# Performance work log

Measured on AMD Instinct MI355X. Metric: run time of the kernel, lower is better.

Reference implementation:

```python
import jax, jax.numpy as jnp
import numpy as np

C = 64
DQK = C // 8  # 8
B, H, W = 1, 128, 128


def setup_inputs() -> dict:
    key = jax.random.key(0)
    ks = jax.random.split(key, 8)
    s = 0.05
    return {
        "x": jax.random.normal(ks[0], (B, C, H, W), dtype=jnp.float32),
        "Wq": jax.random.normal(ks[1], (DQK, C), dtype=jnp.float32) * s,
        "bq": jnp.zeros((DQK,), dtype=jnp.float32),
        "Wk": jax.random.normal(ks[2], (DQK, C), dtype=jnp.float32) * s,
        "bk": jnp.zeros((DQK,), dtype=jnp.float32),
        "Wv": jax.random.normal(ks[3], (C, C), dtype=jnp.float32) * s,
        "bv": jnp.zeros((C,), dtype=jnp.float32),
        "gamma": jnp.ones((1,), dtype=jnp.float32),  # torch inits to 0; nonzero for testing
    }


def reference(x, Wq, bq, Wk, bk, Wv, bv, gamma):
    b, c, h, w = x.shape
    n = h * w
    xf = x.reshape(b, c, n)                      # [B,C,N] (unfold k=1 == reshape)
    q = jnp.einsum('dc,bcn->bnd', Wq, xf) + bq   # [B,N,DQK]
    k = jnp.einsum('dc,bcn->bnd', Wk, xf) + bk   # [B,N,DQK]
    v = jnp.einsum('dc,bcn->bnd', Wv, xf) + bv   # [B,N,C]
    attn = jnp.einsum('bnd,bmd->bnm', q, k)      # [B,N,N] (no scaling, as in source)
    attn = jax.nn.softmax(attn, axis=-1)
    out = jnp.einsum('bnm,bmc->bnc', attn, v)    # [B,N,C]
    out = out.transpose(0, 2, 1).reshape(b, c, h, w)  # fold k=1 == reshape
    return gamma * out + x
```

## Files before the change

kernel.cpp:

```cpp
#include <hip/hip_runtime.h>
#include <stdint.h>

#define NTOK 16384

typedef __attribute__((ext_vector_type(8))) short short8;
typedef __attribute__((ext_vector_type(4))) float f32x4;
typedef __attribute__((ext_vector_type(16))) float f32x16;

__device__ __forceinline__ short f2bf_rne(float f) {
  union { float f; unsigned u; } a; a.f = f;
  unsigned r = a.u + 0x7fffu + ((a.u >> 16) & 1u);
  return (short)(r >> 16);
}

__device__ __forceinline__ float fast_exp2(float x) {
#if __has_builtin(__builtin_amdgcn_exp2f)
  return __builtin_amdgcn_exp2f(x);
#else
  return exp2f(x);
#endif
}

__device__ __forceinline__ unsigned pack_rn(float lo, float hi) {
  union { float f; unsigned u; } a, b;
  a.f = lo; b.f = hi;
  return __builtin_amdgcn_perm(b.u + 0x8000u, a.u + 0x8000u, 0x07060302u);
}

__device__ __forceinline__ int sigma32(int s) {
  int t = (s >> 2) & 3;
  return (t == 1 || t == 2) ? (s ^ 12) : s;
}

__global__ __launch_bounds__(256) void proj_qk_kernel(
    const float* __restrict__ x,
    const float* __restrict__ Wq, const float* __restrict__ bq,
    const float* __restrict__ Wk, const float* __restrict__ bk,
    short* __restrict__ Qp, short* __restrict__ Kp)
{
  __shared__ float sWq[512], sWk[512], sbq[8], sbk[8];
  const int tid = threadIdx.x;
  for (int i = tid; i < 512; i += 256) { sWq[i] = Wq[i]; sWk[i] = Wk[i]; }
  if (tid < 8) { sbq[tid] = bq[tid]; sbk[tid] = bk[tid]; }
  __syncthreads();

  const int n = blockIdx.x * 256 + tid;
  float xv[64];
#pragma unroll
  for (int c = 0; c < 64; ++c) xv[c] = x[c * NTOK + n];

  short8 qv, kv;
#pragma unroll
  for (int d = 0; d < 8; ++d) {
    float qa = sbq[d], ka = sbk[d];
#pragma unroll
    for (int c = 0; c < 64; c += 4) {
      f32x4 wq = *reinterpret_cast<const f32x4*>(&sWq[d * 64 + c]);
      f32x4 wk = *reinterpret_cast<const f32x4*>(&sWk[d * 64 + c]);
      qa += wq[0]*xv[c] + wq[1]*xv[c+1] + wq[2]*xv[c+2] + wq[3]*xv[c+3];
      ka += wk[0]*xv[c] + wk[1]*xv[c+1] + wk[2]*xv[c+2] + wk[3]*xv[c+3];
    }
    qv[d] = f2bf_rne(qa);
    kv[d] = f2bf_rne(ka * 1.44269504f);
  }
  *reinterpret_cast<short8*>(Qp + (size_t)n * 8) = qv;
  const int slot = (n & ~31) | sigma32(n & 31);
  *reinterpret_cast<short8*>(Kp + (size_t)slot * 8) = kv;
}

__global__ __launch_bounds__(256) void proj_v_kernel(
    const float* __restrict__ x,
    const float* __restrict__ Wv, const float* __restrict__ bv,
    short* __restrict__ VF)
{
  __shared__ float sW[64 * 65];
  __shared__ float sx[64][32];
  __shared__ float sb[64];
  const int tid = threadIdx.x;
  const int n0 = blockIdx.x * 32;

  for (int i = tid; i < 4096; i += 256) sW[(i >> 6) * 65 + (i & 63)] = Wv[i];
  if (tid < 64) sb[tid] = bv[tid];
  for (int i = tid; i < 2048; i += 256) {
    const int r = i >> 5, col = i & 31;
    sx[r][col] = x[(size_t)r * NTOK + n0 + col];
  }
  __syncthreads();

  const int c   = tid & 63;
  const int oct = tid >> 6;

  float v[8];
  const float bias = sb[c];
#pragma unroll
  for (int j = 0; j < 8; ++j) v[j] = bias;

  for (int cp = 0; cp < 64; ++cp) {
    const float wv = sW[c * 65 + cp];
    const float* xr = &sx[cp][oct * 8];
#pragma unroll
    for (int j = 0; j < 8; ++j) v[j] += wv * xr[j];
  }

  const int n    = n0 + oct * 8;
  const int frag = (n >> 4) * 2 + (c >> 5);
  const int lane = ((n >> 3) & 1) * 32 + (c & 31);
  short8 ov;
#pragma unroll
  for (int j = 0; j < 8; ++j) ov[j] = f2bf_rne(v[j]);
  *reinterpret_cast<short8*>(VF + (size_t)frag * 512 + lane * 8) = ov;
}

__global__ __launch_bounds__(512, 4) void attn_fused_kernel(
    const short* __restrict__ Qp, const short* __restrict__ Kp,
    const short* __restrict__ VF,
    const float* __restrict__ x, const float* __restrict__ gamma,
    float* __restrict__ out)
{
  __shared__ float lacc[8 * 2080];
  __shared__ float slsum[8 * 32];

  const int tid  = threadIdx.x;
  const int w    = tid >> 6;
  const int lane = tid & 63;
  const int hi   = lane >> 5;
  const int ln   = lane & 31;
  const int q0   = blockIdx.x * 32;

  const short8 zero8 = {0,0,0,0,0,0,0,0};
  f32x16 zf16;
#pragma unroll
  for (int i = 0; i < 16; ++i) zf16[i] = 0.f;

  short8 qf = hi ? zero8
                 : *reinterpret_cast<const short8*>(Qp + (size_t)(q0 + ln) * 8);

  f32x16 acc0 = zf16, acc1 = zf16;
  float lsum = 0.f;

  const int kvlen = NTOK / 8;
  const int kv_lo = w * kvlen;
  const int nh    = kvlen / 32;

  const short* KP0 = Kp + ((size_t)kv_lo + ln) * 8;
  const short* VF0 = VF + (size_t)kv_lo * 64 + lane * 8;

  auto loadK = [&](int h, short8& kf) {
    kf = *reinterpret_cast<const short8*>(KP0 + (size_t)h * 256);
  };
  auto loadV = [&](int h, short8 (&vf)[4]) {
    const short* vp = VF0 + (size_t)h * 2048;
#pragma unroll
    for (int j = 0; j < 4; ++j)
      vf[j] = *reinterpret_cast<const short8*>(vp + j * 512);
  };

  auto expPack = [&](const f32x16& sv, unsigned (&u)[8]) {
    float t[8];
#pragma unroll
    for (int j = 0; j < 8; ++j) {
      float e0 = fast_exp2(sv[2*j]);
      float e1 = fast_exp2(sv[2*j+1]);
      u[j] = pack_rn(e0, e1);
      t[j] = e0 + e1;
    }
    lsum += ((t[0]+t[1]) + (t[2]+t[3])) + ((t[4]+t[5]) + (t[6]+t[7]));
  };

  auto pvHalf = [&](const unsigned (&u)[8], const short8 (&vf)[4]) {
    union { unsigned u32[4]; short8 s8; } pa0, pa1;
#pragma unroll
    for (int j = 0; j < 4; ++j) { pa0.u32[j] = u[j]; pa1.u32[j] = u[4+j]; }
    acc0 = __builtin_amdgcn_mfma_f32_32x32x16_bf16(pa0.s8, vf[0], acc0, 0, 0, 0);
    acc1 = __builtin_amdgcn_mfma_f32_32x32x16_bf16(pa0.s8, vf[1], acc1, 0, 0, 0);
    acc0 = __builtin_amdgcn_mfma_f32_32x32x16_bf16(pa1.s8, vf[2], acc0, 0, 0, 0);
    acc1 = __builtin_amdgcn_mfma_f32_32x32x16_bf16(pa1.s8, vf[3], acc1, 0, 0, 0);
  };

  short8 kA, kB, vA[4], vB[4];
  loadK(0, kA); loadV(0, vA);
  loadK(1, kB); loadV(1, vB);
  f32x16 svA = __builtin_amdgcn_mfma_f32_32x32x16_bf16(kA, qf, zf16, 0, 0, 0);
  f32x16 svB;

  for (int h = 0; h < nh; h += 2) {
    svB = __builtin_amdgcn_mfma_f32_32x32x16_bf16(kB, qf, zf16, 0, 0, 0);
    { const int hp = (h + 2 < nh) ? h + 2 : nh - 1; loadK(hp, kA); }
    unsigned u[8];
    expPack(svA, u);
    pvHalf(u, vA);
    { const int hp = (h + 2 < nh) ? h + 2 : nh - 1; loadV(hp, vA); }

    svA = __builtin_amdgcn_mfma_f32_32x32x16_bf16(kA, qf, zf16, 0, 0, 0);
    { const int hp = (h + 3 < nh) ? h + 3 : nh - 1; loadK(hp, kB); }
    unsigned u2[8];
    expPack(svB, u2);
    pvHalf(u2, vB);
    { const int hp = (h + 3 < nh) ? h + 3 : nh - 1; loadV(hp, vB); }
  }

  float* la = &lacc[w * 2080];
#pragma unroll
  for (int r = 0; r < 16; ++r) {
    const int qrow = (r & 3) + 8 * (r >> 2) + 4 * hi;
    la[qrow * 65 + ln]      = acc0[r];
    la[qrow * 65 + 32 + ln] = acc1[r];
  }
  lsum += __shfl_xor(lsum, 32);
  if (lane < 32) slsum[w * 32 + ln] = lsum;
  __syncthreads();

  const int q = tid & 31;
  float ls = 0.f;
#pragma unroll
  for (int w2 = 0; w2 < 8; ++w2) ls += slsum[w2 * 32 + q];
  const float inv = 1.f / ls;
  const float gam = gamma[0];

#pragma unroll
  for (int k = 0; k < 4; ++k) {
    const int c = (tid >> 5) + k * 16;
    float sum = 0.f;
#pragma unroll
    for (int w2 = 0; w2 < 8; ++w2) sum += lacc[w2 * 2080 + q * 65 + c];
    const size_t idx = (size_t)c * NTOK + q0 + q;
    out[idx] = gam * sum * inv + x[idx];
  }
}

extern "C" void kernel_launch(void* const* d_in, const int* in_sizes, int n_in,
                              void* d_out, int out_size, void* d_ws, size_t ws_size,
                              hipStream_t stream) {
  const float* x     = (const float*)d_in[0];
  const float* Wq    = (const float*)d_in[1];
  const float* bq    = (const float*)d_in[2];
  const float* Wk    = (const float*)d_in[3];
  const float* bk    = (const float*)d_in[4];
  const float* Wv    = (const float*)d_in[5];
  const float* bv    = (const float*)d_in[6];
  const float* gamma = (const float*)d_in[7];
  float* out = (float*)d_out;

  short* Qp = (short*)d_ws;
  short* Kp = Qp + (size_t)NTOK * 8;
  short* VF = Kp + (size_t)NTOK * 8;

  proj_qk_kernel<<<NTOK / 256, 256, 0, stream>>>(x, Wq, bq, Wk, bk, Qp, Kp);
  proj_v_kernel<<<NTOK / 32, 256, 0, stream>>>(x, Wv, bv, VF);
  attn_fused_kernel<<<NTOK / 32, 512, 0, stream>>>(Qp, Kp, VF, x, gamma, out);
}
```

Before: 81.03 us.

## Fuse QK and V projections; compute softmax row sums via MFMA with ones

Merges the Q/K projection into the V projection kernel so x is loaded into shared memory once and one launch is removed. In the attention loop, the per-lane exp row-sum (VALU adds plus a cross-lane shuffle) is replaced by extra MFMAs against a ones vector, so the sums come out of the matrix unit. The bf16 packing of probabilities switches from round-to-nearest to truncation to save instructions. This adds two MFMAs per step and introduces truncation bias, which is consistent between numerator and denominator because both use the same packed values.

```diff
diff --git a/kernel.cpp b/kernel.cpp
--- a/kernel.cpp
+++ b/kernel.cpp
@@ -21,10 +21,10 @@
 #endif
 }
 
-__device__ __forceinline__ unsigned pack_rn(float lo, float hi) {
+__device__ __forceinline__ unsigned pack_trunc(float lo, float hi) {
   union { float f; unsigned u; } a, b;
   a.f = lo; b.f = hi;
-  return __builtin_amdgcn_perm(b.u + 0x8000u, a.u + 0x8000u, 0x07060302u);
+  return __builtin_amdgcn_perm(b.u, a.u, 0x07060302u);
 }
 
 __device__ __forceinline__ int sigma32(int s) {
@@ -32,83 +32,78 @@
   return (t == 1 || t == 2) ? (s ^ 12) : s;
 }
 
-__global__ __launch_bounds__(256) void proj_qk_kernel(
+__global__ __launch_bounds__(256) void proj_all_kernel(
     const float* __restrict__ x,
     const float* __restrict__ Wq, const float* __restrict__ bq,
     const float* __restrict__ Wk, const float* __restrict__ bk,
-    short* __restrict__ Qp, short* __restrict__ Kp)
-{
-  __shared__ float sWq[512], sWk[512], sbq[8], sbk[8];
-  const int tid = threadIdx.x;
-  for (int i = tid; i < 512; i += 256) { sWq[i] = Wq[i]; sWk[i] = Wk[i]; }
-  if (tid < 8) { sbq[tid] = bq[tid]; sbk[tid] = bk[tid]; }
-  __syncthreads();
-
-  const int n = blockIdx.x * 256 + tid;
-  float xv[64];
-#pragma unroll
-  for (int c = 0; c < 64; ++c) xv[c] = x[c * NTOK + n];
-
-  short8 qv, kv;
-#pragma unroll
-  for (int d = 0; d < 8; ++d) {
-    float qa = sbq[d], ka = sbk[d];
-#pragma unroll
-    for (int c = 0; c < 64; c += 4) {
-      f32x4 wq = *reinterpret_cast<const f32x4*>(&sWq[d * 64 + c]);
-      f32x4 wk = *reinterpret_cast<const f32x4*>(&sWk[d * 64 + c]);
-      qa += wq[0]*xv[c] + wq[1]*xv[c+1] + wq[2]*xv[c+2] + wq[3]*xv[c+3];
-      ka += wk[0]*xv[c] + wk[1]*xv[c+1] + wk[2]*xv[c+2] + wk[3]*xv[c+3];
-    }
-    qv[d] = f2bf_rne(qa);
-    kv[d] = f2bf_rne(ka * 1.44269504f);
-  }
-  *reinterpret_cast<short8*>(Qp + (size_t)n * 8) = qv;
-  const int slot = (n & ~31) | sigma32(n & 31);
-  *reinterpret_cast<short8*>(Kp + (size_t)slot * 8) = kv;
-}
-
-__global__ __launch_bounds__(256) void proj_v_kernel(
-    const float* __restrict__ x,
     const float* __restrict__ Wv, const float* __restrict__ bv,
-    short* __restrict__ VF)
+    short* __restrict__ Qp, short* __restrict__ Kp, short* __restrict__ VF)
 {
   __shared__ float sW[64 * 65];
   __shared__ float sx[64][32];
   __shared__ float sb[64];
+  __shared__ float sWqk[16 * 65];
+  __shared__ float sbqk[16];
   const int tid = threadIdx.x;
   const int n0 = blockIdx.x * 32;
 
   for (int i = tid; i < 4096; i += 256) sW[(i >> 6) * 65 + (i & 63)] = Wv[i];
   if (tid < 64) sb[tid] = bv[tid];
+  for (int i = tid; i < 512; i += 256) {
+    sWqk[(i >> 6) * 65 + (i & 63)]       = Wq[i];
+    sWqk[((i >> 6) + 8) * 65 + (i & 63)] = Wk[i];
+  }
+  if (tid < 8)       sbqk[tid] = bq[tid];
+  else if (tid < 16) sbqk[tid] = bk[tid - 8];
   for (int i = tid; i < 2048; i += 256) {
     const int r = i >> 5, col = i & 31;
     sx[r][col] = x[(size_t)r * NTOK + n0 + col];
   }
   __syncthreads();
 
-  const int c   = tid & 63;
-  const int oct = tid >> 6;
-
-  float v[8];
-  const float bias = sb[c];
-#pragma unroll
-  for (int j = 0; j < 8; ++j) v[j] = bias;
-
-  for (int cp = 0; cp < 64; ++cp) {
-    const float wv = sW[c * 65 + cp];
-    const float* xr = &sx[cp][oct * 8];
-#pragma unroll
-    for (int j = 0; j < 8; ++j) v[j] += wv * xr[j];
-  }
-
-  const int n    = n0 + oct * 8;
-  const int frag = (n >> 4) * 2 + (c >> 5);
-  const int lane = ((n >> 3) & 1) * 32 + (c & 31);
-  short8 ov;
-#pragma unroll
-  for (int j = 0; j < 8; ++j) ov[j] = f2bf_rne(v[j]);
-  *reinterpret_cast<short8*>(VF + (size_t)frag * 512 + lane * 8) = ov;
+  {
+    const int c   = tid & 63;
+    const int oct = tid >> 6;
+    float v[8];
+    const float bias = sb[c];
+#pragma unroll
+    for (int j = 0; j < 8; ++j) v[j] = bias;
+    for (int cp = 0; cp < 64; ++cp) {
+      const float wv = sW[c * 65 + cp];
+      const float* xr = &sx[cp][oct * 8];
+#pragma unroll
+      for (int j = 0; j < 8; ++j) v[j] += wv * xr[j];
+    }
+    const int n    = n0 + oct * 8;
+    const int frag = (n >> 4) * 2 + (c >> 5);
+    const int lane = ((n >> 3) & 1) * 32 + (c & 31);
+    short8 ov;
+#pragma unroll
+    for (int j = 0; j < 8; ++j) ov[j] = f2bf_rne(v[j]);
+    *reinterpret_cast<short8*>(VF + (size_t)frag * 512 + lane * 8) = ov;
+  }
+
+  {
+    const int qk = tid & 15;
+    const int tp = tid >> 4;
+    float a0 = 0.f, a1 = 0.f;
+    for (int cp = 0; cp < 64; ++cp) {
+      const float wv = sWqk[qk * 65 + cp];
+      a0 += wv * sx[cp][tp];
+      a1 += wv * sx[cp][tp + 16];
+    }
+    const float bias = sbqk[qk];
+    if (qk < 8) {
+      Qp[(size_t)(n0 + tp) * 8 + qk]      = f2bf_rne(a0 + bias);
+      Qp[(size_t)(n0 + tp + 16) * 8 + qk] = f2bf_rne(a1 + bias);
+    } else {
+      const int d = qk - 8;
+      Kp[(size_t)(n0 + sigma32(tp)) * 8 + d] =
+          f2bf_rne((a0 + bias) * 1.44269504f);
+      Kp[(size_t)(n0 + sigma32(tp + 16)) * 8 + d] =
+          f2bf_rne((a1 + bias) * 1.44269504f);
+    }
+  }
 }
 
 __global__ __launch_bounds__(512, 4) void attn_fused_kernel(
@@ -128,6 +123,8 @@
   const int q0   = blockIdx.x * 32;
 
   const short8 zero8 = {0,0,0,0,0,0,0,0};
+  const short  one_bf = (short)0x3F80;
+  const short8 ones8 = {one_bf,one_bf,one_bf,one_bf,one_bf,one_bf,one_bf,one_bf};
   f32x16 zf16;
 #pragma unroll
   for (int i = 0; i < 16; ++i) zf16[i] = 0.f;
@@ -136,7 +133,7 @@
                  : *reinterpret_cast<const short8*>(Qp + (size_t)(q0 + ln) * 8);
 
   f32x16 acc0 = zf16, acc1 = zf16;
-  float lsum = 0.f;
+  f32x16 acc_l = zf16;
 
   const int kvlen = NTOK / 8;
   const int kv_lo = w * kvlen;
@@ -156,25 +153,24 @@
   };
 
   auto expPack = [&](const f32x16& sv, unsigned (&u)[8]) {
-    float t[8];
 #pragma unroll
     for (int j = 0; j < 8; ++j) {
       float e0 = fast_exp2(sv[2*j]);
       float e1 = fast_exp2(sv[2*j+1]);
-      u[j] = pack_rn(e0, e1);
-      t[j] = e0 + e1;
-    }
-    lsum += ((t[0]+t[1]) + (t[2]+t[3])) + ((t[4]+t[5]) + (t[6]+t[7]));
+      u[j] = pack_trunc(e0, e1);
+    }
   };
 
   auto pvHalf = [&](const unsigned (&u)[8], const short8 (&vf)[4]) {
     union { unsigned u32[4]; short8 s8; } pa0, pa1;
 #pragma unroll
     for (int j = 0; j < 4; ++j) { pa0.u32[j] = u[j]; pa1.u32[j] = u[4+j]; }
-    acc0 = __builtin_amdgcn_mfma_f32_32x32x16_bf16(pa0.s8, vf[0], acc0, 0, 0, 0);
-    acc1 = __builtin_amdgcn_mfma_f32_32x32x16_bf16(pa0.s8, vf[1], acc1, 0, 0, 0);
-    acc0 = __builtin_amdgcn_mfma_f32_32x32x16_bf16(pa1.s8, vf[2], acc0, 0, 0, 0);
-    acc1 = __builtin_amdgcn_mfma_f32_32x32x16_bf16(pa1.s8, vf[3], acc1, 0, 0, 0);
+    acc0  = __builtin_amdgcn_mfma_f32_32x32x16_bf16(pa0.s8, vf[0], acc0, 0, 0, 0);
+    acc1  = __builtin_amdgcn_mfma_f32_32x32x16_bf16(pa0.s8, vf[1], acc1, 0, 0, 0);
+    acc_l = __builtin_amdgcn_mfma_f32_32x32x16_bf16(pa0.s8, ones8, acc_l, 0, 0, 0);
+    acc0  = __builtin_amdgcn_mfma_f32_32x32x16_bf16(pa1.s8, vf[2], acc0, 0, 0, 0);
+    acc1  = __builtin_amdgcn_mfma_f32_32x32x16_bf16(pa1.s8, vf[3], acc1, 0, 0, 0);
+    acc_l = __builtin_amdgcn_mfma_f32_32x32x16_bf16(pa1.s8, ones8, acc_l, 0, 0, 0);
   };
 
   short8 kA, kB, vA[4], vB[4];
@@ -206,8 +202,13 @@
     la[qrow * 65 + ln]      = acc0[r];
     la[qrow * 65 + 32 + ln] = acc1[r];
   }
-  lsum += __shfl_xor(lsum, 32);
-  if (lane < 32) slsum[w * 32 + ln] = lsum;
+  if (ln == 0) {
+#pragma unroll
+    for (int r = 0; r < 16; ++r) {
+      const int qrow = (r & 3) + 8 * (r >> 2) + 4 * hi;
+      slsum[w * 32 + qrow] = acc_l[r];
+    }
+  }
   __syncthreads();
 
   const int q = tid & 31;
@@ -245,7 +246,7 @@
   short* Kp = Qp + (size_t)NTOK * 8;
   short* VF = Kp + (size_t)NTOK * 8;
 
-  proj_qk_kernel<<<NTOK / 256, 256, 0, stream>>>(x, Wq, bq, Wk, bk, Qp, Kp);
-  proj_v_kernel<<<NTOK / 32, 256, 0, stream>>>(x, Wv, bv, VF);
+  proj_all_kernel<<<NTOK / 32, 256, 0, stream>>>(x, Wq, bq, Wk, bk, Wv, bv,
+                                                 Qp, Kp, VF);
   attn_fused_kernel<<<NTOK / 32, 512, 0, stream>>>(Qp, Kp, VF, x, gamma, out);
 }
```

Result: no change. 80.69 us (-0.4%).
